# Performance work log

Measured on AMD Instinct MI355X. Metric: run time of the kernel, lower is better.

The kernel has to match this reference:

```python
import jax, jax.numpy as jnp
import numpy as np

D_IN, D_OUT, K = 256, 512, 64
X_MIN, X_MAX = 0.0, 1.0
EPS = 1e-12


def pchip_slopes(y, x):
    """Fritsch-Carlson PCHIP slopes along last dim. y:(...,K), x:(K,) -> (...,K)."""
    h = x[1:] - x[:-1]                                  # (K-1,)
    delta = (y[..., 1:] - y[..., :-1]) / (h + EPS)      # (...,K-1)

    def limit(di, de):
        di = jnp.where(di * de <= 0, jnp.zeros_like(di), di)
        return jnp.where(jnp.abs(di) > 3 * jnp.abs(de), 3 * de, di)

    d0 = ((2 * h[0] + h[1]) * delta[..., 0] - h[0] * delta[..., 1]) / (h[0] + h[1] + EPS)
    dN = ((2 * h[-1] + h[-2]) * delta[..., -1] - h[-1] * delta[..., -2]) / (h[-1] + h[-2] + EPS)
    dp, dn = delta[..., :-1], delta[..., 1:]
    same_sign = dp * dn > 0
    w1 = 2 * h[1:] + h[:-1]
    w2 = h[1:] + 2 * h[:-1]
    d_int = (w1 + w2) / (w1 / (dp + EPS) + w2 / (dn + EPS) + EPS)
    mid = jnp.where(same_sign, d_int, jnp.zeros_like(d_int))
    return jnp.concatenate([limit(d0, delta[..., 0])[..., None], mid,
                            limit(dN, delta[..., -1])[..., None]], axis=-1)


def kan_forward(x, coeffs, bias, knots):
    """x:(B,d_in), coeffs:(d_out,d_in,K), bias:(d_out,), knots:(K,) -> (B,d_out)."""
    Kn = knots.shape[0]
    d = pchip_slopes(coeffs, knots)                     # (d_out,d_in,K)

    xc = jnp.clip(x, knots[0], knots[-1])
    idx = jnp.clip(jnp.searchsorted(knots, xc) - 1, 0, Kn - 2)   # (B,d_in)
    x0 = knots[idx]
    h = knots[idx + 1] - x0 + EPS
    t = (xc - x0) / h
    t2 = t * t
    t3 = t2 * t
    h00 = 2 * t3 - 3 * t2 + 1
    h10 = t3 - 2 * t2 + t
    h01 = -2 * t3 + 3 * t2
    h11 = t3 - t2

    below = x < knots[0]
    above = x > knots[-1]
    ext = below | above
    # linear extrapolation: value = y_edge + d_edge * (x - knot_edge)
    k0 = jnp.where(below, 0, jnp.where(above, Kn - 1, idx))
    k1 = jnp.where(ext, k0, idx + 1)                    # dummy (zero-weight) index when extrapolating
    dx_ext = jnp.where(below, x - knots[0], x - knots[-1])
    a_y0 = jnp.where(ext, jnp.ones_like(h00), h00)
    a_y1 = jnp.where(ext, jnp.zeros_like(h01), h01)
    a_d0 = jnp.where(ext, dx_ext, h10 * h)
    a_d1 = jnp.where(ext, jnp.zeros_like(h11), h11 * h)

    oh0 = jax.nn.one_hot(k0, Kn, dtype=x.dtype)         # (B,d_in,K)
    oh1 = jax.nn.one_hot(k1, Kn, dtype=x.dtype)
    Wy = a_y0[..., None] * oh0 + a_y1[..., None] * oh1  # weights applied to knot values
    Wd = a_d0[..., None] * oh0 + a_d1[..., None] * oh1  # weights applied to knot slopes

    out = (jnp.einsum('bik,oik->bo', Wy, coeffs)
           + jnp.einsum('bik,oik->bo', Wd, d)
           + bias[None, :])
    return out


def setup_inputs() -> dict:
    key = jax.random.key(0)
    k1, k2 = jax.random.split(key)
    B = 4096
    x = jax.random.uniform(k1, (B, D_IN), dtype=jnp.float32)
    init_scale = 0.1 / np.sqrt(D_IN)
    coeffs = jax.random.normal(k2, (D_OUT, D_IN, K), dtype=jnp.float32) * init_scale
    bias = jnp.zeros((D_OUT,), dtype=jnp.float32)
    knots = jnp.linspace(X_MIN, X_MAX, K, dtype=jnp.float32)
    return {"x": x, "coeffs": coeffs, "bias": bias, "knots": knots}


def reference(x, coeffs, bias, knots):
    return kan_forward(x, coeffs, bias, knots)
```

## Files before the change

### kernel.cpp

```cpp
#include <hip/hip_runtime.h>
#include <hip/hip_fp16.h>
#include <cstdint>

#define D_IN   256
#define D_OUT  512
#define KK     64
#define BATCH  4096
#define EPSF   1e-12f
#define BT     256


using half2v = _Float16 __attribute__((ext_vector_type(2)));

__device__ __forceinline__ float dot2(uint32_t a, uint32_t b, float c) {
#if defined(__has_builtin) && __has_builtin(__builtin_amdgcn_fdot2)
  return __builtin_amdgcn_fdot2(__builtin_bit_cast(half2v, a),
                                __builtin_bit_cast(half2v, b), c, false);
#else
  __half2 ah = __builtin_bit_cast(__half2, a);
  __half2 bh = __builtin_bit_cast(__half2, b);
  return c + __half2float(ah.x) * __half2float(bh.x)
           + __half2float(ah.y) * __half2float(bh.y);
#endif
}

__device__ __forceinline__ uint32_t packh2(float a, float b) {
  __half2 h = __floats2half2_rn(a, b);
  return __builtin_bit_cast(uint32_t, h);
}


__global__ __launch_bounds__(256)
void kan_prep(const float* __restrict__ coeffs, const float* __restrict__ knots,
              const float* __restrict__ x,
              uint32_t* __restrict__ pk2p, uint2* __restrict__ W8,
              unsigned char* __restrict__ K0) {
  __shared__ float s_kn[KK];
  __shared__ float s_h[KK];
  const int bid = blockIdx.x;
  const int tid = threadIdx.x;

  if (bid < 512) {
    if (tid < KK) s_kn[tid] = knots[tid];
    __syncthreads();
    if (tid < KK - 1) s_h[tid] = s_kn[tid + 1] - s_kn[tid];
    __syncthreads();

    const int i = bid >> 1;
    const int o = (bid & 1) * 256 + tid;
    const float* C = coeffs + ((size_t)o * D_IN + i) * KK;

    float c[KK];
#pragma unroll
    for (int k = 0; k < KK; k += 4) {
      float4 v = *(const float4*)(C + k);
      c[k] = v.x; c[k + 1] = v.y; c[k + 2] = v.z; c[k + 3] = v.w;
    }

    float d[KK];
    float h0 = s_h[0], h1 = s_h[1];
    float del0 = (c[1] - c[0]) / (h0 + EPSF);
    float del1 = (c[2] - c[1]) / (h1 + EPSF);
    {
      float di = ((2.f * h0 + h1) * del0 - h0 * del1) / (h0 + h1 + EPSF);
      di = (di * del0 <= 0.f) ? 0.f : di;
      di = (fabsf(di) > 3.f * fabsf(del0)) ? 3.f * del0 : di;
      d[0] = di;
    }
    float dp = del0, dn = del1;
#pragma unroll
    for (int k = 1; k <= KK - 2; ++k) {
      float hk = s_h[k], hkm = s_h[k - 1];
      float w1 = 2.f * hk + hkm;
      float w2 = hk + 2.f * hkm;
      float dint = (w1 + w2) / (w1 / (dp + EPSF) + w2 / (dn + EPSF) + EPSF);
      d[k] = (dp * dn > 0.f) ? dint : 0.f;
      if (k < KK - 2) {
        float nd = (c[k + 2] - c[k + 1]) / (s_h[k + 1] + EPSF);
        dp = dn; dn = nd;
      }
    }
    {
      float hN = s_h[KK - 2], hNm = s_h[KK - 3];
      float di = ((2.f * hN + hNm) * dn - hN * dp) / (hN + hNm + EPSF);
      di = (di * dn <= 0.f) ? 0.f : di;
      di = (fabsf(di) > 3.f * fabsf(dn)) ? 3.f * dn : di;
      d[KK - 1] = di;
    }

    const int oq = o >> 7, og = o & 127;
#pragma unroll
    for (int k = 0; k < KK; ++k) {
      float hk = ((k < KK - 1) ? s_h[k] : s_h[KK - 2]) + EPSF;
      pk2p[((size_t)(((i << 2) + oq) << 6) + k) * 128 + og] = packh2(c[k], d[k] * hk);
    }
  } else {
    const int i = bid - 512;
    const float inv63 = 1.0f / 63.0f;
    for (int b = tid; b < BATCH; b += 256) {
      float xv = x[(size_t)b * D_IN + i];
      float xc = fminf(fmaxf(xv, 0.f), 1.f);
      int k0 = (int)(xc * 63.0f);
      k0 = min(k0, KK - 2);
      float x0 = (float)k0 * inv63;
      if (xc < x0)                              { k0--; x0 -= inv63; }
      else if (k0 < KK - 2 && xc >= x0 + inv63) { k0++; x0 += inv63; }
      float t  = (xc - x0) * 63.0f;
      float t2 = t * t;
      float t3 = t2 * t;
      float wy0 = 2.f * t3 - 3.f * t2 + 1.f;
      float wy1 = 3.f * t2 - 2.f * t3;
      float wd0 = t3 - 2.f * t2 + t;
      float wd1 = t3 - t2;
      uint2 w;
      w.x = packh2(wy0, wd0);
      w.y = packh2(wy1, wd1);
      W8[(size_t)i * BATCH + b] = w;
      K0[(size_t)i * BATCH + b] = (unsigned char)k0;
    }
  }
}


template<int LG>
__global__ __launch_bounds__(1024, 8)
void kan_main(const uint2* __restrict__ W8, const unsigned char* __restrict__ K0,
              const uint4* __restrict__ pkq, __half* __restrict__ P) {
  __shared__ uint4 sb[2][2048];

  const int CIk   = D_IN >> LG;
  const int bid   = blockIdx.x;
  const int chunk = bid & ((1 << LG) - 1);
  const int rest  = bid >> LG;
  const int oq    = rest & 3;
  const int btile = rest >> 2;
  const int tid   = threadIdx.x;
  const int g     = tid & 31;
  const int s     = tid >> 5;
  const int bbase = btile * BT + s * 8;
  const int i0    = chunk * CIk;

  float acc[8][4];
#pragma unroll
  for (int j = 0; j < 8; ++j)
#pragma unroll
    for (int m = 0; m < 4; ++m) acc[j][m] = 0.f;

  uint64_t k8 = *(const uint64_t*)(K0 + (size_t)i0 * BATCH + bbase);
  {
    const uint4* src = pkq + ((size_t)((i0 << 2) + oq) << 11);
    uint4 r0 = src[tid], r1 = src[tid + 1024];
    sb[0][tid] = r0; sb[0][tid + 1024] = r1;
  }
  __syncthreads();

  for (int ic = 0; ic < CIk; ++ic) {
    const int cur = ic & 1;
    const int i   = i0 + ic;
    const bool more = (ic + 1 < CIk);

    uint4 r0, r1;
    uint64_t k8n = 0;
    if (more) {
      const uint4* src = pkq + ((size_t)(((i + 1) << 2) + oq) << 11);
      r0 = src[tid]; r1 = src[tid + 1024];
      k8n = *(const uint64_t*)(K0 + (size_t)(i + 1) * BATCH + bbase);
    }

    uint4 wreg[4];
    const uint4* wp = (const uint4*)(W8 + (size_t)i * BATCH + bbase);
#pragma unroll
    for (int n = 0; n < 4; ++n) wreg[n] = wp[n];

    const uint4* bufc = sb[cur];
#pragma unroll
    for (int j = 0; j < 8; ++j) {
      const uint32_t k0 = (uint32_t)(k8 >> (8 * j)) & 0xFFu;
      const uint4* p = bufc + k0 * 32 + g;
      uint4 q0 = p[0];
      uint4 q1 = p[32];
      uint4 t  = wreg[j >> 1];
      uint32_t w0 = (j & 1) ? t.z : t.x;
      uint32_t w1 = (j & 1) ? t.w : t.y;
      acc[j][0] = dot2(q0.x, w0, acc[j][0]); acc[j][0] = dot2(q1.x, w1, acc[j][0]);
      acc[j][1] = dot2(q0.y, w0, acc[j][1]); acc[j][1] = dot2(q1.y, w1, acc[j][1]);
      acc[j][2] = dot2(q0.z, w0, acc[j][2]); acc[j][2] = dot2(q1.z, w1, acc[j][2]);
      acc[j][3] = dot2(q0.w, w0, acc[j][3]); acc[j][3] = dot2(q1.w, w1, acc[j][3]);
    }

    if (more) {
      uint4* bufn = sb[cur ^ 1];
      bufn[tid] = r0; bufn[tid + 1024] = r1;
      k8 = k8n;
    }
    __syncthreads();
  }

  const size_t pb = ((size_t)chunk * BATCH + bbase) * D_OUT + oq * 128 + g * 4;
#pragma unroll
  for (int j = 0; j < 8; ++j) {
    uint2 h;
    h.x = packh2(acc[j][0], acc[j][1]);
    h.y = packh2(acc[j][2], acc[j][3]);
    *(uint2*)((char*)P + (pb + (size_t)j * D_OUT) * 2) = h;
  }
}


__global__ __launch_bounds__(256)
void kan_reduce(const __half* __restrict__ P, const float* __restrict__ bias,
                float* __restrict__ out, int nchunk) {
  const size_t t = (size_t)blockIdx.x * 256 + threadIdx.x;
  const int o4 = (int)(t & 127);
  float4 sum = ((const float4*)bias)[o4];
  for (int c = 0; c < nchunk; ++c) {
    uint2 h = *(const uint2*)((const char*)P +
              ((size_t)c * BATCH * D_OUT + t * 4) * 2);
    __half2 h01 = __builtin_bit_cast(__half2, h.x);
    __half2 h23 = __builtin_bit_cast(__half2, h.y);
    sum.x += __half2float(h01.x); sum.y += __half2float(h01.y);
    sum.z += __half2float(h23.x); sum.w += __half2float(h23.y);
  }
  ((float4*)out)[t] = sum;
}


extern "C" void kernel_launch(void* const* d_in, const int* in_sizes, int n_in,
                              void* d_out, int out_size, void* d_ws, size_t ws_size,
                              hipStream_t stream) {
  const float* x      = (const float*)d_in[0];
  const float* coeffs = (const float*)d_in[1];
  const float* bias   = (const float*)d_in[2];
  const float* knots  = (const float*)d_in[3];
  float* out = (float*)d_out;

  const size_t pk_bytes = (size_t)D_IN * KK * D_OUT * 4;
  const size_t w_bytes  = (size_t)D_IN * BATCH * 8;
  const size_t k_bytes  = (size_t)D_IN * BATCH;
  const size_t fixed    = pk_bytes + w_bytes + k_bytes;
  const size_t p_one    = (size_t)BATCH * D_OUT * 2;

  int lg = 3;
  if (ws_size < fixed + (p_one << 3)) lg = 2;
  if (ws_size < fixed + (p_one << lg)) return;
  const int nchunk = 1 << lg;

  char* ws = (char*)d_ws;
  uint32_t*      pk2p = (uint32_t*)ws;
  uint2*         W8   = (uint2*)(ws + pk_bytes);
  unsigned char* K0   = (unsigned char*)(ws + pk_bytes + w_bytes);
  __half*        P    = (__half*)(ws + fixed);

  kan_prep<<<dim3(768), 256, 0, stream>>>(coeffs, knots, x, pk2p, W8, K0);
  if (lg == 3)
    kan_main<3><<<dim3(16 * 4 * 8), 1024, 0, stream>>>(W8, K0, (const uint4*)pk2p, P);
  else
    kan_main<2><<<dim3(16 * 4 * 4), 1024, 0, stream>>>(W8, K0, (const uint4*)pk2p, P);
  kan_reduce<<<dim3(BATCH * D_OUT / 4 / 256), 256, 0, stream>>>(P, bias, out, nchunk);
}
```

Before: 126.6 us.

## Stage coefficient tiles via global_load_lds and widen reduce loads to 16 bytes

Replaces the register round-trip for double-buffered coefficient tiles with direct global-to-LDS asynchronous loads, freeing registers and removing the LDS store after compute. The reduce kernel now processes eight outputs per thread with 16-byte loads, halving its thread count. This relies on correct wait/barrier semantics for the async LDS writes.

```diff
diff --git a/kernel.cpp b/kernel.cpp
--- a/kernel.cpp
+++ b/kernel.cpp
@@ -27,6 +27,13 @@
 __device__ __forceinline__ uint32_t packh2(float a, float b) {
   __half2 h = __floats2half2_rn(a, b);
   return __builtin_bit_cast(uint32_t, h);
+}
+
+__device__ __forceinline__ void stage16(const void* g, void* l) {
+  __builtin_amdgcn_global_load_lds(
+      (const __attribute__((address_space(1))) unsigned int*)g,
+      (__attribute__((address_space(3))) unsigned int*)l,
+      16, 0, 0);
 }
 
 
@@ -137,6 +144,7 @@
   const int tid   = threadIdx.x;
   const int g     = tid & 31;
   const int s     = tid >> 5;
+  const int wv    = tid >> 6;
   const int bbase = btile * BT + s * 8;
   const int i0    = chunk * CIk;
 
@@ -149,8 +157,8 @@
   uint64_t k8 = *(const uint64_t*)(K0 + (size_t)i0 * BATCH + bbase);
   {
     const uint4* src = pkq + ((size_t)((i0 << 2) + oq) << 11);
-    uint4 r0 = src[tid], r1 = src[tid + 1024];
-    sb[0][tid] = r0; sb[0][tid + 1024] = r1;
+    stage16(src + tid,        &sb[0][wv * 64]);
+    stage16(src + tid + 1024, &sb[0][1024 + wv * 64]);
   }
   __syncthreads();
 
@@ -159,11 +167,12 @@
     const int i   = i0 + ic;
     const bool more = (ic + 1 < CIk);
 
-    uint4 r0, r1;
     uint64_t k8n = 0;
     if (more) {
       const uint4* src = pkq + ((size_t)(((i + 1) << 2) + oq) << 11);
-      r0 = src[tid]; r1 = src[tid + 1024];
+      uint4* bufn = sb[cur ^ 1];
+      stage16(src + tid,        bufn + wv * 64);
+      stage16(src + tid + 1024, bufn + 1024 + wv * 64);
       k8n = *(const uint64_t*)(K0 + (size_t)(i + 1) * BATCH + bbase);
     }
 
@@ -188,11 +197,7 @@
       acc[j][3] = dot2(q0.w, w0, acc[j][3]); acc[j][3] = dot2(q1.w, w1, acc[j][3]);
     }
 
-    if (more) {
-      uint4* bufn = sb[cur ^ 1];
-      bufn[tid] = r0; bufn[tid + 1024] = r1;
-      k8 = k8n;
-    }
+    k8 = k8n;
     __syncthreads();
   }
 
@@ -208,20 +213,26 @@
 
 
 __global__ __launch_bounds__(256)
-void kan_reduce(const __half* __restrict__ P, const float* __restrict__ bias,
-                float* __restrict__ out, int nchunk) {
+void kan_reduce(const uint4* __restrict__ P4, const float* __restrict__ bias,
+                float4* __restrict__ out4, int nchunk) {
   const size_t t = (size_t)blockIdx.x * 256 + threadIdx.x;
-  const int o4 = (int)(t & 127);
-  float4 sum = ((const float4*)bias)[o4];
+  const int o8 = (int)(t & 63);
+  float4 s0 = ((const float4*)bias)[o8 * 2];
+  float4 s1 = ((const float4*)bias)[o8 * 2 + 1];
+  const size_t stride = (size_t)BATCH * D_OUT / 8;
   for (int c = 0; c < nchunk; ++c) {
-    uint2 h = *(const uint2*)((const char*)P +
-              ((size_t)c * BATCH * D_OUT + t * 4) * 2);
-    __half2 h01 = __builtin_bit_cast(__half2, h.x);
-    __half2 h23 = __builtin_bit_cast(__half2, h.y);
-    sum.x += __half2float(h01.x); sum.y += __half2float(h01.y);
-    sum.z += __half2float(h23.x); sum.w += __half2float(h23.y);
-  }
-  ((float4*)out)[t] = sum;
+    uint4 h = P4[(size_t)c * stride + t];
+    __half2 a = __builtin_bit_cast(__half2, h.x);
+    __half2 b = __builtin_bit_cast(__half2, h.y);
+    __half2 cc = __builtin_bit_cast(__half2, h.z);
+    __half2 d = __builtin_bit_cast(__half2, h.w);
+    s0.x += __half2float(a.x);  s0.y += __half2float(a.y);
+    s0.z += __half2float(b.x);  s0.w += __half2float(b.y);
+    s1.x += __half2float(cc.x); s1.y += __half2float(cc.y);
+    s1.z += __half2float(d.x);  s1.w += __half2float(d.y);
+  }
+  out4[t * 2]     = s0;
+  out4[t * 2 + 1] = s1;
 }
 
 
@@ -256,5 +267,6 @@
     kan_main<3><<<dim3(16 * 4 * 8), 1024, 0, stream>>>(W8, K0, (const uint4*)pk2p, P);
   else
     kan_main<2><<<dim3(16 * 4 * 4), 1024, 0, stream>>>(W8, K0, (const uint4*)pk2p, P);
-  kan_reduce<<<dim3(BATCH * D_OUT / 4 / 256), 256, 0, stream>>>(P, bias, out, nchunk);
-}
+  kan_reduce<<<dim3(BATCH * D_OUT / 8 / 256), 256, 0, stream>>>(
+      (const uint4*)P, bias, (float4*)out, nchunk);
+}
```

New measurement: 116.3 us. -8.1%, faster.
